# Optimization experiments

Measured on AMD Instinct MI355X. Metric: run time of the kernel, lower is better.

The kernel has to match this reference:

```python
import jax, jax.numpy as jnp
import numpy as np

N, E, D, L = 50000, 800000, 128, 3  # nodes, edges, feature dim, layers
BN_EPS = 1e-5


def setup_inputs() -> dict:
    key = jax.random.key(0)
    ks = jax.random.split(key, 6)
    x = jax.random.normal(ks[0], (N, D), dtype=jnp.float32)
    edge_index = jax.random.randint(ks[1], (2, E), 0, N, dtype=jnp.int64)
    eps = jnp.zeros((L,), dtype=jnp.float32)
    # Linear weights ~ fan-in scaled init for numerical sanity
    W1 = jax.random.normal(ks[2], (L, D, D), dtype=jnp.float32) * (1.0 / np.sqrt(D))
    b1 = jnp.zeros((L, D), dtype=jnp.float32)
    W2 = jax.random.normal(ks[3], (L, D, D), dtype=jnp.float32) * (1.0 / np.sqrt(D))
    b2 = jnp.zeros((L, D), dtype=jnp.float32)
    bn1_g = jnp.ones((L, D), dtype=jnp.float32)
    bn1_b = jnp.zeros((L, D), dtype=jnp.float32)
    bn2_g = jnp.ones((L, D), dtype=jnp.float32)
    bn2_b = jnp.zeros((L, D), dtype=jnp.float32)
    return {"x": x, "edge_index": edge_index, "eps": eps, "W1": W1, "b1": b1,
            "bn1_g": bn1_g, "bn1_b": bn1_b, "W2": W2, "b2": b2,
            "bn2_g": bn2_g, "bn2_b": bn2_b}


def _batchnorm(h, g, b):
    # training-mode BatchNorm1d over node axis
    mu = h.mean(axis=0)
    var = h.var(axis=0)
    return (h - mu) * jax.lax.rsqrt(var + BN_EPS) * g + b


def reference(x, edge_index, eps, W1, b1, bn1_g, bn1_b, W2, b2, bn2_g, bn2_b):
    src = edge_index[0]
    dst = edge_index[1]
    h = x
    for l in range(L):
        # message: relu(x_j) gathered per edge; aggregate: scatter-add at dst
        agg = jax.ops.segment_sum(jax.nn.relu(h[src]), dst, num_segments=N)
        z = (1.0 + eps[l]) * h + agg
        # GINConv.mlp: Linear -> BN -> ReLU -> Linear
        z = _batchnorm(z @ W1[l] + b1[l], bn1_g[l], bn1_b[l])
        z = jax.nn.relu(z) @ W2[l] + b2[l]
        # outer per-layer BatchNorm
        z = _batchnorm(z, bn2_g[l], bn2_b[l])
        # ReLU on all but last layer (dropout is identity in eval)
        h = jax.nn.relu(z) if l < L - 1 else z
    return h
```

## Files before the change

### kernel.cpp

```cpp
#include <hip/hip_runtime.h>

#define N_NODES 50000
#define DIM 128
#define BN_EPS 1e-5f

typedef short bf16x8 __attribute__((ext_vector_type(8)));
typedef float f32x4 __attribute__((ext_vector_type(4)));

__device__ __forceinline__ unsigned short f2bf(float x) {
  unsigned u = __float_as_uint(x);
  u += 0x7FFFu + ((u >> 16) & 1u);
  return (unsigned short)(u >> 16);
}
__device__ __forceinline__ float bf2f(unsigned short h) {
  return __uint_as_float(((unsigned)h) << 16);
}

__global__ __launch_bounds__(256) void edge_hist(const int* __restrict__ dst,
                                                 int* __restrict__ cnt, int E) {
  const int e = blockIdx.x * blockDim.x + threadIdx.x;
  if (e < E) atomicAdd(&cnt[dst[e]], 1);
}

__global__ __launch_bounds__(1024) void edge_scan(const int* __restrict__ cnt,
                                                  int* __restrict__ row_ptr) {
  __shared__ int part[1024];
  const int tid = threadIdx.x;
  const int per = (N_NODES + 1023) / 1024;
  const int start = tid * per;
  const int end = min(start + per, N_NODES);
  int s = 0;
  for (int i = start; i < end; ++i) s += cnt[i];
  part[tid] = s;
  __syncthreads();
  for (int off = 1; off < 1024; off <<= 1) {
    const int v = part[tid];
    const int u = (tid >= off) ? part[tid - off] : 0;
    __syncthreads();
    part[tid] = v + u;
    __syncthreads();
  }
  int run = (tid == 0) ? 0 : part[tid - 1];
  for (int i = start; i < end; ++i) {
    row_ptr[i] = run;
    run += cnt[i];
  }
  if (tid == 1023) row_ptr[N_NODES] = run;
}

__global__ __launch_bounds__(256) void edge_fill(const int* __restrict__ src,
                                                 const int* __restrict__ dst,
                                                 const int* __restrict__ row_ptr,
                                                 int* __restrict__ cur,
                                                 int* __restrict__ srcl, int E) {
  const int e = blockIdx.x * blockDim.x + threadIdx.x;
  if (e < E) {
    const int d = dst[e];
    const int pos = row_ptr[d] + atomicAdd(&cur[d], 1);
    srcl[pos] = src[e];
  }
}

template <int FUSE>
__global__ __launch_bounds__(256) void aggregate_combine(
    const float* __restrict__ h, const int* __restrict__ rp,
    const int* __restrict__ srcl, const float* __restrict__ eps_l,
    const float* __restrict__ ac, float* __restrict__ z) {
  const int node =
      __builtin_amdgcn_readfirstlane(blockIdx.x * 4 + (threadIdx.x >> 6));
  if (node >= N_NODES) return;
  const int lane = threadIdx.x & 63;
  const int col = lane * 2;

  float2 av, cv;
  if (FUSE) {
    av.x = ac[col]; av.y = ac[col + 1];
    cv.x = ac[DIM + col]; cv.y = ac[DIM + col + 1];
  }
  const float epsv = 1.0f + *eps_l;

  float2 acc;
  {
    const float2 u =
        *reinterpret_cast<const float2*>(h + (size_t)node * DIM + col);
    float2 s;
    if (FUSE) {
      s.x = fmaxf(fmaf(av.x, u.x, cv.x), 0.f);
      s.y = fmaxf(fmaf(av.y, u.y, cv.y), 0.f);
    } else {
      s = u;
    }
    acc.x = epsv * s.x;
    acc.y = epsv * s.y;
  }

  int p = rp[node];
  const int pe = rp[node + 1];
  for (; p + 8 <= pe; p += 8) {
    int s[8];
#pragma unroll
    for (int i = 0; i < 8; ++i) s[i] = srcl[p + i];
    float2 v[8];
#pragma unroll
    for (int i = 0; i < 8; ++i)
      v[i] = *reinterpret_cast<const float2*>(h + (size_t)s[i] * DIM + col);
#pragma unroll
    for (int i = 0; i < 8; ++i) {
      float mx, my;
      if (FUSE) {
        mx = fmaxf(fmaf(av.x, v[i].x, cv.x), 0.f);
        my = fmaxf(fmaf(av.y, v[i].y, cv.y), 0.f);
      } else {
        mx = fmaxf(v[i].x, 0.f);
        my = fmaxf(v[i].y, 0.f);
      }
      acc.x += mx;
      acc.y += my;
    }
  }
  for (; p < pe; ++p) {
    const int s = srcl[p];
    const float2 v =
        *reinterpret_cast<const float2*>(h + (size_t)s * DIM + col);
    if (FUSE) {
      acc.x += fmaxf(fmaf(av.x, v.x, cv.x), 0.f);
      acc.y += fmaxf(fmaf(av.y, v.y, cv.y), 0.f);
    } else {
      acc.x += fmaxf(v.x, 0.f);
      acc.y += fmaxf(v.y, 0.f);
    }
  }
  *reinterpret_cast<float2*>(z + (size_t)node * DIM + col) = acc;
}

__global__ __launch_bounds__(256) void prep_w(const float* __restrict__ W,
                                              unsigned short* __restrict__ hi,
                                              unsigned short* __restrict__ lo) {
  const int idx = blockIdx.x * 256 + threadIdx.x;
  const int i = idx & 7;
  const int l = (idx >> 3) & 63;
  const int t = (idx >> 9) & 7;
  const int s = idx >> 12;
  const int k = s * 32 + ((l >> 4) << 3) + i;
  const int j = t * 16 + (l & 15);
  const float v = W[k * DIM + j];
  const unsigned short h = f2bf(v);
  hi[idx] = h;
  lo[idx] = f2bf(v - bf2f(h));
}

template <int MODE>
__global__ __launch_bounds__(256, 2) void gemm_mfma(
    const float* __restrict__ in, const float* __restrict__ ac,
    const unsigned short* __restrict__ whi,
    const unsigned short* __restrict__ wlo, const float* __restrict__ bias,
    float* __restrict__ out, float* __restrict__ stats) {
  const int tid = threadIdx.x;
  const int lane = tid & 63;
  const int wv = tid >> 6;
  const int rbase = blockIdx.x * 128 + wv * 32;
  const int lr = lane & 15;
  const int lk = (lane >> 4) << 3;

  f32x4 acc[2][8];
#pragma unroll
  for (int m = 0; m < 2; ++m)
#pragma unroll
    for (int t = 0; t < 8; ++t) acc[m][t] = (f32x4)(0.f);

  const int r0 = min(rbase + lr, N_NODES - 1);
  const int r1 = min(rbase + 16 + lr, N_NODES - 1);
  const float* __restrict__ z0 = in + (size_t)r0 * DIM + lk;
  const float* __restrict__ z1 = in + (size_t)r1 * DIM + lk;
  const bf16x8* __restrict__ bh = (const bf16x8*)whi + lane;
  const bf16x8* __restrict__ bl = (const bf16x8*)wlo + lane;

#pragma unroll 1
  for (int s = 0; s < 4; ++s) {
    const int k0 = s * 32;
    float a0v[8], a1v[8];
    {
      const float4 p0 = *reinterpret_cast<const float4*>(z0 + k0);
      const float4 p1 = *reinterpret_cast<const float4*>(z0 + k0 + 4);
      a0v[0] = p0.x; a0v[1] = p0.y; a0v[2] = p0.z; a0v[3] = p0.w;
      a0v[4] = p1.x; a0v[5] = p1.y; a0v[6] = p1.z; a0v[7] = p1.w;
      const float4 q0 = *reinterpret_cast<const float4*>(z1 + k0);
      const float4 q1 = *reinterpret_cast<const float4*>(z1 + k0 + 4);
      a1v[0] = q0.x; a1v[1] = q0.y; a1v[2] = q0.z; a1v[3] = q0.w;
      a1v[4] = q1.x; a1v[5] = q1.y; a1v[6] = q1.z; a1v[7] = q1.w;
    }
    if (MODE == 1) {
      const float4 A0 = *reinterpret_cast<const float4*>(ac + k0 + lk);
      const float4 A1 = *reinterpret_cast<const float4*>(ac + k0 + lk + 4);
      const float4 C0 = *reinterpret_cast<const float4*>(ac + DIM + k0 + lk);
      const float4 C1 =
          *reinterpret_cast<const float4*>(ac + DIM + k0 + lk + 4);
      float aa[8], cc[8];
      aa[0] = A0.x; aa[1] = A0.y; aa[2] = A0.z; aa[3] = A0.w;
      aa[4] = A1.x; aa[5] = A1.y; aa[6] = A1.z; aa[7] = A1.w;
      cc[0] = C0.x; cc[1] = C0.y; cc[2] = C0.z; cc[3] = C0.w;
      cc[4] = C1.x; cc[5] = C1.y; cc[6] = C1.z; cc[7] = C1.w;
#pragma unroll
      for (int i = 0; i < 8; ++i) {
        a0v[i] = fmaxf(fmaf(aa[i], a0v[i], cc[i]), 0.f);
        a1v[i] = fmaxf(fmaf(aa[i], a1v[i], cc[i]), 0.f);
      }
    }
    bf16x8 ah0, al0, ah1, al1;
#pragma unroll
    for (int i = 0; i < 8; ++i) {
      unsigned short h = f2bf(a0v[i]);
      ah0[i] = (short)h;
      al0[i] = (short)f2bf(a0v[i] - bf2f(h));
      h = f2bf(a1v[i]);
      ah1[i] = (short)h;
      al1[i] = (short)f2bf(a1v[i] - bf2f(h));
    }
#pragma unroll
    for (int t = 0; t < 8; ++t) {
      const bf16x8 bhv = bh[(s * 8 + t) * 64];
      const bf16x8 blv = bl[(s * 8 + t) * 64];
      acc[0][t] =
          __builtin_amdgcn_mfma_f32_16x16x32_bf16(ah0, bhv, acc[0][t], 0, 0, 0);
      acc[0][t] =
          __builtin_amdgcn_mfma_f32_16x16x32_bf16(al0, bhv, acc[0][t], 0, 0, 0);
      acc[0][t] =
          __builtin_amdgcn_mfma_f32_16x16x32_bf16(ah0, blv, acc[0][t], 0, 0, 0);
      acc[1][t] =
          __builtin_amdgcn_mfma_f32_16x16x32_bf16(ah1, bhv, acc[1][t], 0, 0, 0);
      acc[1][t] =
          __builtin_amdgcn_mfma_f32_16x16x32_bf16(al1, bhv, acc[1][t], 0, 0, 0);
      acc[1][t] =
          __builtin_amdgcn_mfma_f32_16x16x32_bf16(ah1, blv, acc[1][t], 0, 0, 0);
    }
  }

  float bj[8];
#pragma unroll
  for (int t = 0; t < 8; ++t) bj[t] = bias[t * 16 + lr];
  float cs[8], cq[8];
#pragma unroll
  for (int t = 0; t < 8; ++t) { cs[t] = 0.f; cq[t] = 0.f; }
#pragma unroll
  for (int m = 0; m < 2; ++m) {
    const int rb2 = rbase + m * 16 + ((lane >> 4) << 2);
#pragma unroll
    for (int t = 0; t < 8; ++t) {
#pragma unroll
      for (int j = 0; j < 4; ++j) {
        const int rr = rb2 + j;
        const float v = acc[m][t][j] + bj[t];
        if (rr < N_NODES) {
          out[(size_t)rr * DIM + t * 16 + lr] = v;
          cs[t] += v;
          cq[t] += v * v;
        }
      }
    }
  }
#pragma unroll
  for (int t = 0; t < 8; ++t) {
    cs[t] += __shfl_xor(cs[t], 16);
    cs[t] += __shfl_xor(cs[t], 32);
    cq[t] += __shfl_xor(cq[t], 16);
    cq[t] += __shfl_xor(cq[t], 32);
  }
  if (lane < 16) {
#pragma unroll
    for (int t = 0; t < 8; ++t) {
      atomicAdd(&stats[t * 16 + lane], cs[t]);
      atomicAdd(&stats[DIM + t * 16 + lane], cq[t]);
    }
  }
}

__global__ void bn_param(const float* __restrict__ stats,
                         const float* __restrict__ g,
                         const float* __restrict__ b, float* __restrict__ ac) {
  const int j = threadIdx.x;
  const float invN = 1.0f / (float)N_NODES;
  const float mu = stats[j] * invN;
  const float var = stats[DIM + j] * invN - mu * mu;
  const float a = g[j] * rsqrtf(var + BN_EPS);
  ac[j] = a;
  ac[DIM + j] = b[j] - mu * a;
}

__global__ __launch_bounds__(256) void apply_bn(const float* __restrict__ t,
                                                const float* __restrict__ ac,
                                                float* __restrict__ out) {
  const int i = blockIdx.x * blockDim.x + threadIdx.x;
  const int k = (i * 4) & (DIM - 1);
  const float4 v = *reinterpret_cast<const float4*>(&t[(size_t)i * 4]);
  const float4 a = *reinterpret_cast<const float4*>(&ac[k]);
  const float4 c = *reinterpret_cast<const float4*>(&ac[DIM + k]);
  float4 r;
  r.x = fmaf(a.x, v.x, c.x);
  r.y = fmaf(a.y, v.y, c.y);
  r.z = fmaf(a.z, v.z, c.z);
  r.w = fmaf(a.w, v.w, c.w);
  *reinterpret_cast<float4*>(&out[(size_t)i * 4]) = r;
}

extern "C" void kernel_launch(void* const* d_in, const int* in_sizes, int n_in,
                              void* d_out, int out_size, void* d_ws,
                              size_t ws_size, hipStream_t stream) {
  const float* x = (const float*)d_in[0];
  const int* ei = (const int*)d_in[1];
  const float* eps = (const float*)d_in[2];
  const float* W1 = (const float*)d_in[3];
  const float* b1 = (const float*)d_in[4];
  const float* g1 = (const float*)d_in[5];
  const float* bb1 = (const float*)d_in[6];
  const float* W2 = (const float*)d_in[7];
  const float* b2 = (const float*)d_in[8];
  const float* g2 = (const float*)d_in[9];
  const float* bb2 = (const float*)d_in[10];

  const int E = in_sizes[1] / 2;
  const size_t ND = (size_t)N_NODES * DIM;

  float* bufA = (float*)d_ws;
  float* bufB = bufA + ND;
  float* stats = bufB + ND;
  float* bnp = stats + 512;
  int* cnt = (int*)(bnp + 512);
  int* row_ptr = cnt + N_NODES;
  int* cur = row_ptr + N_NODES + 1;
  int* srcl = cur + N_NODES;
  unsigned short* wf = (unsigned short*)(srcl + E);

  const int edge_grid = (E + 255) / 256;
  const int agg_grid = (N_NODES + 3) / 4;
  const int gemm_grid = (N_NODES + 127) / 128;
  const int apply_grid = (N_NODES * DIM / 4) / 256;

  for (int l = 0; l < 3; ++l) {
    unsigned short* f1 = wf + (size_t)(2 * l) * 32768;
    unsigned short* f2 = wf + (size_t)(2 * l + 1) * 32768;
    prep_w<<<64, 256, 0, stream>>>(W1 + (size_t)l * DIM * DIM, f1, f1 + 16384);
    prep_w<<<64, 256, 0, stream>>>(W2 + (size_t)l * DIM * DIM, f2, f2 + 16384);
  }

  hipMemsetAsync(cnt, 0, sizeof(int) * (size_t)N_NODES, stream);
  hipMemsetAsync(cur, 0, sizeof(int) * (size_t)N_NODES, stream);
  edge_hist<<<edge_grid, 256, 0, stream>>>(ei + E, cnt, E);
  edge_scan<<<1, 1024, 0, stream>>>(cnt, row_ptr);
  edge_fill<<<edge_grid, 256, 0, stream>>>(ei, ei + E, row_ptr, cur, srcl, E);

  const float* hin = x;
  float* zb = bufA;
  float* tb = bufB;
  for (int l = 0; l < 3; ++l) {
    unsigned short* f1 = wf + (size_t)(2 * l) * 32768;
    unsigned short* f2 = wf + (size_t)(2 * l + 1) * 32768;
    hipMemsetAsync(stats, 0, sizeof(float) * 512, stream);
    if (l == 0)
      aggregate_combine<0><<<agg_grid, 256, 0, stream>>>(hin, row_ptr, srcl,
                                                         eps + l, nullptr, zb);
    else
      aggregate_combine<1><<<agg_grid, 256, 0, stream>>>(
          hin, row_ptr, srcl, eps + l, bnp + 256, zb);
    gemm_mfma<2><<<gemm_grid, 256, 0, stream>>>(zb, nullptr, f1, f1 + 16384,
                                                b1 + l * DIM, tb, stats);
    bn_param<<<1, DIM, 0, stream>>>(stats, g1 + l * DIM, bb1 + l * DIM, bnp);
    gemm_mfma<1><<<gemm_grid, 256, 0, stream>>>(tb, bnp, f2, f2 + 16384,
                                                b2 + l * DIM, zb, stats + 256);
    bn_param<<<1, DIM, 0, stream>>>(stats + 256, g2 + l * DIM, bb2 + l * DIM,
                                    bnp + 256);
    hin = zb;
    float* tmp = zb;
    zb = tb;
    tb = tmp;
  }
  apply_bn<<<apply_grid, 256, 0, stream>>>(hin, bnp + 256, (float*)d_out);
}
```

Before: 834.2 us.

## Parallelize CSR scan and fold BN parameter computation into consumer kernels

Replaces the single-block serial prefix scan over node degrees with a three-kernel multi-block scan (block-local scan, block-sum scan, offset add). Removes the tiny bn_param kernels by having the aggregate, GEMM and final apply kernels compute the BN scale and shift directly from the accumulated stats. Per-layer stats buffers are also zeroed with one memset up front instead of one per layer. This cuts serialized launches and the slow single-block scan, in exchange for redundant rsqrt work in every consumer thread and two extra small scan launches.

```diff
diff --git a/kernel.cpp b/kernel.cpp
--- a/kernel.cpp
+++ b/kernel.cpp
@@ -3,6 +3,7 @@
 #define N_NODES 50000
 #define DIM 128
 #define BN_EPS 1e-5f
+#define SCAN_B 49
 
 typedef short bf16x8 __attribute__((ext_vector_type(8)));
 typedef float f32x4 __attribute__((ext_vector_type(4)));
@@ -22,30 +23,71 @@
   if (e < E) atomicAdd(&cnt[dst[e]], 1);
 }
 
-__global__ __launch_bounds__(1024) void edge_scan(const int* __restrict__ cnt,
-                                                  int* __restrict__ row_ptr) {
-  __shared__ int part[1024];
+__global__ __launch_bounds__(256) void scan1(const int* __restrict__ cnt,
+                                             int* __restrict__ row_ptr,
+                                             int* __restrict__ bsum) {
+  __shared__ int lds[256];
   const int tid = threadIdx.x;
-  const int per = (N_NODES + 1023) / 1024;
-  const int start = tid * per;
-  const int end = min(start + per, N_NODES);
-  int s = 0;
-  for (int i = start; i < end; ++i) s += cnt[i];
-  part[tid] = s;
+  const int base = blockIdx.x * 1024 + tid * 4;
+  int v0 = 0, v1 = 0, v2 = 0, v3 = 0;
+  if (base + 3 < N_NODES) {
+    const int4 c4 = *reinterpret_cast<const int4*>(cnt + base);
+    v0 = c4.x; v1 = c4.y; v2 = c4.z; v3 = c4.w;
+  } else if (base < N_NODES) {
+    v0 = cnt[base];
+    if (base + 1 < N_NODES) v1 = cnt[base + 1];
+    if (base + 2 < N_NODES) v2 = cnt[base + 2];
+    if (base + 3 < N_NODES) v3 = cnt[base + 3];
+  }
+  lds[tid] = v0 + v1 + v2 + v3;
   __syncthreads();
-  for (int off = 1; off < 1024; off <<= 1) {
-    const int v = part[tid];
-    const int u = (tid >= off) ? part[tid - off] : 0;
+  for (int off = 1; off < 256; off <<= 1) {
+    const int val = lds[tid];
+    const int add = (tid >= off) ? lds[tid - off] : 0;
     __syncthreads();
-    part[tid] = v + u;
+    lds[tid] = val + add;
     __syncthreads();
   }
-  int run = (tid == 0) ? 0 : part[tid - 1];
-  for (int i = start; i < end; ++i) {
-    row_ptr[i] = run;
-    run += cnt[i];
-  }
-  if (tid == 1023) row_ptr[N_NODES] = run;
+  const int pre = tid ? lds[tid - 1] : 0;
+  if (base < N_NODES) {
+    row_ptr[base] = pre;
+    if (base + 1 < N_NODES) row_ptr[base + 1] = pre + v0;
+    if (base + 2 < N_NODES) row_ptr[base + 2] = pre + v0 + v1;
+    if (base + 3 < N_NODES) row_ptr[base + 3] = pre + v0 + v1 + v2;
+  }
+  if (tid == 255) bsum[blockIdx.x] = lds[255];
+}
+
+__global__ __launch_bounds__(64) void scan2(const int* __restrict__ bsum,
+                                            int* __restrict__ boff,
+                                            int* __restrict__ row_ptr_tail) {
+  __shared__ int lds[64];
+  const int t = threadIdx.x;
+  const int v = (t < SCAN_B) ? bsum[t] : 0;
+  lds[t] = v;
+  __syncthreads();
+  for (int off = 1; off < 64; off <<= 1) {
+    const int val = lds[t];
+    const int add = (t >= off) ? lds[t - off] : 0;
+    __syncthreads();
+    lds[t] = val + add;
+    __syncthreads();
+  }
+  if (t < SCAN_B) boff[t] = lds[t] - v;
+  if (t == SCAN_B - 1) row_ptr_tail[0] = lds[t];
+}
+
+__global__ __launch_bounds__(256) void scan3(int* __restrict__ row_ptr,
+                                             const int* __restrict__ boff) {
+  const int i = blockIdx.x * 1024 + threadIdx.x * 4;
+  const int off = boff[blockIdx.x];
+  if (i + 3 < N_NODES) {
+    int4 r = *reinterpret_cast<int4*>(row_ptr + i);
+    r.x += off; r.y += off; r.z += off; r.w += off;
+    *reinterpret_cast<int4*>(row_ptr + i) = r;
+  } else if (i < N_NODES) {
+    for (int k = i; k < N_NODES; ++k) row_ptr[k] += off;
+  }
 }
 
 __global__ __launch_bounds__(256) void edge_fill(const int* __restrict__ src,
@@ -65,7 +107,8 @@
 __global__ __launch_bounds__(256) void aggregate_combine(
     const float* __restrict__ h, const int* __restrict__ rp,
     const int* __restrict__ srcl, const float* __restrict__ eps_l,
-    const float* __restrict__ ac, float* __restrict__ z) {
+    const float* __restrict__ st, const float* __restrict__ gg,
+    const float* __restrict__ bg, float* __restrict__ z) {
   const int node =
       __builtin_amdgcn_readfirstlane(blockIdx.x * 4 + (threadIdx.x >> 6));
   if (node >= N_NODES) return;
@@ -74,8 +117,15 @@
 
   float2 av, cv;
   if (FUSE) {
-    av.x = ac[col]; av.y = ac[col + 1];
-    cv.x = ac[DIM + col]; cv.y = ac[DIM + col + 1];
+    const float invN = 1.0f / (float)N_NODES;
+    const float mu0 = st[col] * invN;
+    const float mu1 = st[col + 1] * invN;
+    const float va0 = fmaf(-mu0, mu0, st[DIM + col] * invN);
+    const float va1 = fmaf(-mu1, mu1, st[DIM + col + 1] * invN);
+    av.x = gg[col] * rsqrtf(va0 + BN_EPS);
+    av.y = gg[col + 1] * rsqrtf(va1 + BN_EPS);
+    cv.x = fmaf(-mu0, av.x, bg[col]);
+    cv.y = fmaf(-mu1, av.y, bg[col + 1]);
   }
   const float epsv = 1.0f + *eps_l;
 
@@ -151,7 +201,8 @@
 
 template <int MODE>
 __global__ __launch_bounds__(256, 2) void gemm_mfma(
-    const float* __restrict__ in, const float* __restrict__ ac,
+    const float* __restrict__ in, const float* __restrict__ ist,
+    const float* __restrict__ ig, const float* __restrict__ ib,
     const unsigned short* __restrict__ whi,
     const unsigned short* __restrict__ wlo, const float* __restrict__ bias,
     float* __restrict__ out, float* __restrict__ stats) {
@@ -190,20 +241,33 @@
       a1v[4] = q1.x; a1v[5] = q1.y; a1v[6] = q1.z; a1v[7] = q1.w;
     }
     if (MODE == 1) {
-      const float4 A0 = *reinterpret_cast<const float4*>(ac + k0 + lk);
-      const float4 A1 = *reinterpret_cast<const float4*>(ac + k0 + lk + 4);
-      const float4 C0 = *reinterpret_cast<const float4*>(ac + DIM + k0 + lk);
-      const float4 C1 =
-          *reinterpret_cast<const float4*>(ac + DIM + k0 + lk + 4);
-      float aa[8], cc[8];
-      aa[0] = A0.x; aa[1] = A0.y; aa[2] = A0.z; aa[3] = A0.w;
-      aa[4] = A1.x; aa[5] = A1.y; aa[6] = A1.z; aa[7] = A1.w;
-      cc[0] = C0.x; cc[1] = C0.y; cc[2] = C0.z; cc[3] = C0.w;
-      cc[4] = C1.x; cc[5] = C1.y; cc[6] = C1.z; cc[7] = C1.w;
+      const float invN = 1.0f / (float)N_NODES;
+      const float4 S0 = *reinterpret_cast<const float4*>(ist + k0 + lk);
+      const float4 S1 = *reinterpret_cast<const float4*>(ist + k0 + lk + 4);
+      const float4 Q0 = *reinterpret_cast<const float4*>(ist + DIM + k0 + lk);
+      const float4 Q1 =
+          *reinterpret_cast<const float4*>(ist + DIM + k0 + lk + 4);
+      const float4 G0 = *reinterpret_cast<const float4*>(ig + k0 + lk);
+      const float4 G1 = *reinterpret_cast<const float4*>(ig + k0 + lk + 4);
+      const float4 B0 = *reinterpret_cast<const float4*>(ib + k0 + lk);
+      const float4 B1 = *reinterpret_cast<const float4*>(ib + k0 + lk + 4);
+      float ss[8], qq[8], gv[8], bv[8];
+      ss[0] = S0.x; ss[1] = S0.y; ss[2] = S0.z; ss[3] = S0.w;
+      ss[4] = S1.x; ss[5] = S1.y; ss[6] = S1.z; ss[7] = S1.w;
+      qq[0] = Q0.x; qq[1] = Q0.y; qq[2] = Q0.z; qq[3] = Q0.w;
+      qq[4] = Q1.x; qq[5] = Q1.y; qq[6] = Q1.z; qq[7] = Q1.w;
+      gv[0] = G0.x; gv[1] = G0.y; gv[2] = G0.z; gv[3] = G0.w;
+      gv[4] = G1.x; gv[5] = G1.y; gv[6] = G1.z; gv[7] = G1.w;
+      bv[0] = B0.x; bv[1] = B0.y; bv[2] = B0.z; bv[3] = B0.w;
+      bv[4] = B1.x; bv[5] = B1.y; bv[6] = B1.z; bv[7] = B1.w;
 #pragma unroll
       for (int i = 0; i < 8; ++i) {
-        a0v[i] = fmaxf(fmaf(aa[i], a0v[i], cc[i]), 0.f);
-        a1v[i] = fmaxf(fmaf(aa[i], a1v[i], cc[i]), 0.f);
+        const float mu = ss[i] * invN;
+        const float var = fmaf(-mu, mu, qq[i] * invN);
+        const float a = gv[i] * rsqrtf(var + BN_EPS);
+        const float c = fmaf(-mu, a, bv[i]);
+        a0v[i] = fmaxf(fmaf(a, a0v[i], c), 0.f);
+        a1v[i] = fmaxf(fmaf(a, a1v[i], c), 0.f);
       }
     }
     bf16x8 ah0, al0, ah1, al1;
@@ -274,31 +338,40 @@
   }
 }
 
-__global__ void bn_param(const float* __restrict__ stats,
-                         const float* __restrict__ g,
-                         const float* __restrict__ b, float* __restrict__ ac) {
-  const int j = threadIdx.x;
-  const float invN = 1.0f / (float)N_NODES;
-  const float mu = stats[j] * invN;
-  const float var = stats[DIM + j] * invN - mu * mu;
-  const float a = g[j] * rsqrtf(var + BN_EPS);
-  ac[j] = a;
-  ac[DIM + j] = b[j] - mu * a;
-}
-
 __global__ __launch_bounds__(256) void apply_bn(const float* __restrict__ t,
-                                                const float* __restrict__ ac,
+                                                const float* __restrict__ st,
+                                                const float* __restrict__ gg,
+                                                const float* __restrict__ bg,
                                                 float* __restrict__ out) {
   const int i = blockIdx.x * blockDim.x + threadIdx.x;
   const int k = (i * 4) & (DIM - 1);
+  const float invN = 1.0f / (float)N_NODES;
+  const float4 S = *reinterpret_cast<const float4*>(&st[k]);
+  const float4 Q = *reinterpret_cast<const float4*>(&st[DIM + k]);
+  const float4 G = *reinterpret_cast<const float4*>(&gg[k]);
+  const float4 B = *reinterpret_cast<const float4*>(&bg[k]);
   const float4 v = *reinterpret_cast<const float4*>(&t[(size_t)i * 4]);
-  const float4 a = *reinterpret_cast<const float4*>(&ac[k]);
-  const float4 c = *reinterpret_cast<const float4*>(&ac[DIM + k]);
   float4 r;
-  r.x = fmaf(a.x, v.x, c.x);
-  r.y = fmaf(a.y, v.y, c.y);
-  r.z = fmaf(a.z, v.z, c.z);
-  r.w = fmaf(a.w, v.w, c.w);
+  {
+    const float mu = S.x * invN;
+    const float a = G.x * rsqrtf(fmaf(-mu, mu, Q.x * invN) + BN_EPS);
+    r.x = fmaf(a, v.x, fmaf(-mu, a, B.x));
+  }
+  {
+    const float mu = S.y * invN;
+    const float a = G.y * rsqrtf(fmaf(-mu, mu, Q.y * invN) + BN_EPS);
+    r.y = fmaf(a, v.y, fmaf(-mu, a, B.y));
+  }
+  {
+    const float mu = S.z * invN;
+    const float a = G.z * rsqrtf(fmaf(-mu, mu, Q.z * invN) + BN_EPS);
+    r.z = fmaf(a, v.z, fmaf(-mu, a, B.z));
+  }
+  {
+    const float mu = S.w * invN;
+    const float a = G.w * rsqrtf(fmaf(-mu, mu, Q.w * invN) + BN_EPS);
+    r.w = fmaf(a, v.w, fmaf(-mu, a, B.w));
+  }
   *reinterpret_cast<float4*>(&out[(size_t)i * 4]) = r;
 }
 
@@ -323,12 +396,13 @@
   float* bufA = (float*)d_ws;
   float* bufB = bufA + ND;
   float* stats = bufB + ND;
-  float* bnp = stats + 512;
-  int* cnt = (int*)(bnp + 512);
+  unsigned short* wf = (unsigned short*)(stats + 1536);
+  int* cnt = (int*)(wf + 6 * 32768);
   int* row_ptr = cnt + N_NODES;
   int* cur = row_ptr + N_NODES + 1;
   int* srcl = cur + N_NODES;
-  unsigned short* wf = (unsigned short*)(srcl + E);
+  int* bsum = srcl + E;
+  int* boff = bsum + 64;
 
   const int edge_grid = (E + 255) / 256;
   const int agg_grid = (N_NODES + 3) / 4;
@@ -344,8 +418,11 @@
 
   hipMemsetAsync(cnt, 0, sizeof(int) * (size_t)N_NODES, stream);
   hipMemsetAsync(cur, 0, sizeof(int) * (size_t)N_NODES, stream);
+  hipMemsetAsync(stats, 0, sizeof(float) * 1536, stream);
   edge_hist<<<edge_grid, 256, 0, stream>>>(ei + E, cnt, E);
-  edge_scan<<<1, 1024, 0, stream>>>(cnt, row_ptr);
+  scan1<<<SCAN_B, 256, 0, stream>>>(cnt, row_ptr, bsum);
+  scan2<<<1, 64, 0, stream>>>(bsum, boff, row_ptr + N_NODES);
+  scan3<<<SCAN_B, 256, 0, stream>>>(row_ptr, boff);
   edge_fill<<<edge_grid, 256, 0, stream>>>(ei, ei + E, row_ptr, cur, srcl, E);
 
   const float* hin = x;
@@ -354,24 +431,25 @@
   for (int l = 0; l < 3; ++l) {
     unsigned short* f1 = wf + (size_t)(2 * l) * 32768;
     unsigned short* f2 = wf + (size_t)(2 * l + 1) * 32768;
-    hipMemsetAsync(stats, 0, sizeof(float) * 512, stream);
+    float* stL = stats + l * 512;
     if (l == 0)
-      aggregate_combine<0><<<agg_grid, 256, 0, stream>>>(hin, row_ptr, srcl,
-                                                         eps + l, nullptr, zb);
+      aggregate_combine<0><<<agg_grid, 256, 0, stream>>>(
+          hin, row_ptr, srcl, eps + l, nullptr, nullptr, nullptr, zb);
     else
       aggregate_combine<1><<<agg_grid, 256, 0, stream>>>(
-          hin, row_ptr, srcl, eps + l, bnp + 256, zb);
-    gemm_mfma<2><<<gemm_grid, 256, 0, stream>>>(zb, nullptr, f1, f1 + 16384,
-                                                b1 + l * DIM, tb, stats);
-    bn_param<<<1, DIM, 0, stream>>>(stats, g1 + l * DIM, bb1 + l * DIM, bnp);
-    gemm_mfma<1><<<gemm_grid, 256, 0, stream>>>(tb, bnp, f2, f2 + 16384,
-                                                b2 + l * DIM, zb, stats + 256);
-    bn_param<<<1, DIM, 0, stream>>>(stats + 256, g2 + l * DIM, bb2 + l * DIM,
-                                    bnp + 256);
+          hin, row_ptr, srcl, eps + l, stats + (l - 1) * 512 + 256,
+          g2 + (l - 1) * DIM, bb2 + (l - 1) * DIM, zb);
+    gemm_mfma<2><<<gemm_grid, 256, 0, stream>>>(
+        zb, nullptr, nullptr, nullptr, f1, f1 + 16384, b1 + l * DIM, tb, stL);
+    gemm_mfma<1><<<gemm_grid, 256, 0, stream>>>(
+        tb, stL, g1 + l * DIM, bb1 + l * DIM, f2, f2 + 16384, b2 + l * DIM, zb,
+        stL + 256);
     hin = zb;
     float* tmp = zb;
     zb = tb;
     tb = tmp;
   }
-  apply_bn<<<apply_grid, 256, 0, stream>>>(hin, bnp + 256, (float*)d_out);
-}
+  apply_bn<<<apply_grid, 256, 0, stream>>>(hin, stats + 2 * 512 + 256,
+                                           g2 + 2 * DIM, bb2 + 2 * DIM,
+                                           (float*)d_out);
+}
```

After: 765.5 us. -8.2%, faster.
